# Optimization experiments

Hardware: AMD Instinct MI355X
Metric: run time of the kernel (lower is better)

## Reference

```python
import jax, jax.numpy as jnp
import numpy as np

T_STEPS = 64      # AR order p
MAX_T = 65536     # trajectory length
BATCH = 256       # number of sampled trajectories
STD = 0.3


def setup_inputs() -> dict:
    key = jax.random.key(0)
    k1, k2, k3 = jax.random.split(key, 3)
    raw = jax.random.normal(k1, (T_STEPS,), dtype=jnp.float32)
    # torch init: params / sum(|params|)
    params = raw / jnp.sum(jnp.abs(raw))
    bias = jax.random.uniform(k2, (1,), dtype=jnp.float32)
    noise = jax.random.normal(k3, (BATCH, MAX_T), dtype=jnp.float32)
    return {"params": params, "bias": bias, "noise": noise}


def _ar_means(params, bias, length):
    """AR(p) recurrence: mean_i = sum_k params[k] * x[i-1-k] + bias, x init = 0.
    State holds the last p values, most-recent-first (matches the reversed
    indexing inputs[i-1 : i-p-1 : -1] in the torch code)."""
    p = params.shape[0]

    def step(state, _):
        new = jnp.dot(state, params) + bias[0]
        state = jnp.concatenate([new[None], state[:-1]])
        return state, new

    init = jnp.zeros((p,), dtype=params.dtype)
    _, means = jax.lax.scan(step, init, None, length=length)
    return means  # [length]


def reference(params, bias, noise):
    # means of the Normal over the trajectory (deterministic, shared by batch)
    means = _ar_means(params, bias, noise.shape[1])  # [T]
    # reparameterized sample: actions = mean + std * eps, eps ~ N(0, 1)
    actions = means[None, :] + jnp.asarray(STD, noise.dtype) * noise  # [B, T]
    return actions
```

## Files before the change

### kernel.cpp

```cpp
#include <hip/hip_runtime.h>

#define T_LEN   65536
#define BATCH   256
#define P       64
#define BASE    4096
#define K1_THREADS 256
#define W_TILE  1024
#define BCHUNK  8
#define VOFF    65536

typedef float f4 __attribute__((ext_vector_type(4)));


__constant__ int SCH_DST[14] = { 2, 3, 4, 6, 5, 7, 8,10,12,14, 9,11,13,15};
__constant__ int SCH_SRC[14] = { 1, 2, 2, 3, 4, 6, 4, 5, 6, 7, 8,10,12,14};
__constant__ int SCH_DBL[14] = { 1, 0, 1, 1, 0, 0, 1, 1, 1, 1, 0, 0, 0, 0};
__constant__ int SCH_W[14]   = {192,256,128,192,256,256,64,192,128,192,256,256,256,256};

__global__ __launch_bounds__(K1_THREADS, 1) void ar_k1(const float* __restrict__ params,
                                                       float* __restrict__ R) {
    __shared__ __align__(16) float Rl[BASE];
    __shared__ float p[128];
    __shared__ float Wp[64][4];
    __shared__ __align__(16) float Vs[68];
    __shared__ __align__(16) float Vnode[16][68];
    __shared__ __align__(16) float Tn[8][256];
    __shared__ __align__(16) float Ts[256];
    const int tid = threadIdx.x;
    if (tid < 128) p[tid] = (tid < P) ? params[tid] : 0.f;
    __syncthreads();

    if (tid < 64) {
        float z = 0.f;
        const float pk = p[tid];
        for (int t = 0; t < 64; ++t) {
            float y  = __shfl(z, 0) + 1.0f;
            float zn = __shfl_down(z, 1);
            if (tid == 63) zn = 0.f;
            z = fmaf(pk, y, zn);
            if (tid == 0) Rl[t] = y;
        }
    }
    __syncthreads();

    for (int L = 64; L <= BASE / 2; L <<= 1) {
        {
            const int j = tid >> 2, c = tid & 3;
            const int mbase = c << 4;
            float w = 0.f;
            #pragma unroll
            for (int mm = 0; mm < 16; ++mm) {
                const int m = mbase + mm;
                w = fmaf(p[m + j], Rl[L - 1 - m], w);
            }
            Wp[j][c] = w;
        }
        __syncthreads();
        if (tid <= P) {
            const float wj  = (tid < P)
                ? (Wp[tid][0] + Wp[tid][1] + Wp[tid][2] + Wp[tid][3]) : 0.f;
            const float wm1 = (tid >= 1)
                ? (Wp[tid-1][0] + Wp[tid-1][1] + Wp[tid-1][2] + Wp[tid-1][3]) : 0.f;
            Vs[tid] = wj - wm1;
        }
        __syncthreads();
        if (tid < P) {
            const int tau = tid;
            float acc = Rl[tau];
            #pragma unroll
            for (int i = 0; i < P; ++i) {
                const int idx = (tau - i) > 0 ? (tau - i) : 0;
                const float v = (i <= tau) ? Vs[i] : 0.f;
                acc = fmaf(v, Rl[idx], acc);
            }
            Rl[L + tau] = acc;
        }
        {
            const f4* __restrict__ Rl4 = reinterpret_cast<const f4*>(Rl);
            f4* __restrict__ Rl4w = reinterpret_cast<f4*>(Rl);
            const f4* __restrict__ V4 = reinterpret_cast<const f4*>(Vs);
            const int nq = (L - 64) >> 2;
            #pragma unroll 1
            for (int q = tid; q < nq; q += K1_THREADS) {
                f4 w4[17];
                #pragma unroll
                for (int j = 0; j < 17; ++j) w4[j] = Rl4[q + j];
                float a0 = w4[16].x, a1 = w4[16].y, a2 = w4[16].z, a3 = w4[16].w;
                #pragma unroll
                for (int g = 0; g < 16; ++g) {
                    const f4 v  = V4[g];
                    const f4 hi = w4[16 - g];
                    const f4 lo = w4[15 - g];
                    a0 = fmaf(v.x, hi.x, a0); a1 = fmaf(v.x, hi.y, a1);
                    a2 = fmaf(v.x, hi.z, a2); a3 = fmaf(v.x, hi.w, a3);
                    a0 = fmaf(v.y, lo.w, a0); a1 = fmaf(v.y, hi.x, a1);
                    a2 = fmaf(v.y, hi.y, a2); a3 = fmaf(v.y, hi.z, a3);
                    a0 = fmaf(v.z, lo.z, a0); a1 = fmaf(v.z, lo.w, a1);
                    a2 = fmaf(v.z, hi.x, a2); a3 = fmaf(v.z, hi.y, a3);
                    a0 = fmaf(v.w, lo.y, a0); a1 = fmaf(v.w, lo.z, a1);
                    a2 = fmaf(v.w, lo.w, a2); a3 = fmaf(v.w, hi.x, a3);
                }
                const float v64 = Vs[64];
                a0 = fmaf(v64, w4[0].x, a0); a1 = fmaf(v64, w4[0].y, a1);
                a2 = fmaf(v64, w4[0].z, a2); a3 = fmaf(v64, w4[0].w, a3);
                f4 o; o.x = a0; o.y = a1; o.z = a2; o.w = a3;
                Rl4w[((L + 64) >> 2) + q] = o;
            }
        }
        __syncthreads();
    }

    for (int j = tid; j < BASE / 4; j += K1_THREADS)
        reinterpret_cast<f4*>(R)[j] = reinterpret_cast<const f4*>(Rl)[j];

    Tn[1][tid] = Rl[3840 + tid];
    __syncthreads();
    {
        const int j = tid >> 2, c = tid & 3, mbase = c << 4;
        float w = 0.f;
        #pragma unroll
        for (int mm = 0; mm < 16; ++mm) {
            const int m = mbase + mm;
            w = fmaf(p[m + j], Tn[1][255 - m], w);
        }
        Wp[j][c] = w;
    }
    __syncthreads();
    if (tid <= P) {
        const float wj  = (tid < P)
            ? (Wp[tid][0] + Wp[tid][1] + Wp[tid][2] + Wp[tid][3]) : 0.f;
        const float wm1 = (tid >= 1)
            ? (Wp[tid-1][0] + Wp[tid-1][1] + Wp[tid-1][2] + Wp[tid-1][3]) : 0.f;
        Vnode[1][tid] = wj - wm1;
    }
    __syncthreads();

    for (int s = 0; s < 14; ++s) {
        const int dst = SCH_DST[s], src = SCH_SRC[s], wd = SCH_W[s];
        const bool dbl = SCH_DBL[s] != 0;
        float* td = (dst <= 7) ? Tn[dst] : Ts;
        const float* tsrc = Tn[src];
        const float* Vsr  = Vnode[src];
        if (tid < wd) {
            const float* s0 = dbl ? (tsrc + 64) : (Rl + 3840);
            float acc = s0[tid];
            #pragma unroll
            for (int i = 0; i <= P; ++i)
                acc = fmaf(Vsr[i], s0[tid - i], acc);
            td[tid] = acc;
        }
        __syncthreads();
        {
            const int j = tid >> 2, c = tid & 3, mbase = c << 4;
            float w = 0.f;
            #pragma unroll
            for (int mm = 0; mm < 16; ++mm) {
                const int m = mbase + mm;
                w = fmaf(p[m + j], td[wd - 1 - m], w);
            }
            Wp[j][c] = w;
        }
        __syncthreads();
        if (tid <= P) {
            const float wj  = (tid < P)
                ? (Wp[tid][0] + Wp[tid][1] + Wp[tid][2] + Wp[tid][3]) : 0.f;
            const float wm1 = (tid >= 1)
                ? (Wp[tid-1][0] + Wp[tid-1][1] + Wp[tid-1][2] + Wp[tid-1][3]) : 0.f;
            Vnode[dst][tid] = wj - wm1;
        }
        __syncthreads();
    }

    for (int j = tid; j < 15 * 80; j += K1_THREADS) {
        const int k = j / 80 + 1, i = j - (k - 1) * 80;
        if (i < 65) R[VOFF + k * 80 + i] = Vnode[k][i];
    }
}

__global__ __launch_bounds__(256) void ar_out_fused(const float* __restrict__ R,
                                                    const float* __restrict__ bias,
                                                    const float* __restrict__ noise,
                                                    float* __restrict__ out) {
    __shared__ __align__(16) float win[1088];
    __shared__ __align__(16) float Vl[68];
    const int tid  = threadIdx.x;
    const int tile = blockIdx.x & 63;
    const int bc   = blockIdx.x >> 6;
    const int t0   = tile * W_TILE;
    const float b  = bias[0];
    const int k    = t0 >> 12;
    const f4* __restrict__ Rg4 = reinterpret_cast<const f4*>(R);

    f4 rt;
    if (k == 0) {
        const f4 r = Rg4[(t0 >> 2) + tid];
        rt.x = b * r.x; rt.y = b * r.y; rt.z = b * r.z; rt.w = b * r.w;
    } else {
        const int tau0 = t0 & 4095;
        if (tid < 65) Vl[tid] = R[VOFF + k * 80 + tid];
        f4* __restrict__ win4 = reinterpret_cast<f4*>(win);
        for (int j4 = tid; j4 < 272; j4 += 256) {
            const int u = tau0 - 64 + 4 * j4;
            f4 v;
            if (u >= 0) v = Rg4[u >> 2];
            else { v.x = 0.f; v.y = 0.f; v.z = 0.f; v.w = 0.f; }
            win4[j4] = v;
        }
        __syncthreads();
        const f4* __restrict__ V4 = reinterpret_cast<const f4*>(Vl);
        f4 w4[17];
        #pragma unroll
        for (int j = 0; j < 17; ++j) w4[j] = win4[tid + j];
        float a0 = w4[16].x, a1 = w4[16].y, a2 = w4[16].z, a3 = w4[16].w;
        #pragma unroll
        for (int g = 0; g < 16; ++g) {
            const f4 v  = V4[g];
            const f4 hi = w4[16 - g];
            const f4 lo = w4[15 - g];
            a0 = fmaf(v.x, hi.x, a0); a1 = fmaf(v.x, hi.y, a1);
            a2 = fmaf(v.x, hi.z, a2); a3 = fmaf(v.x, hi.w, a3);
            a0 = fmaf(v.y, lo.w, a0); a1 = fmaf(v.y, hi.x, a1);
            a2 = fmaf(v.y, hi.y, a2); a3 = fmaf(v.y, hi.z, a3);
            a0 = fmaf(v.z, lo.z, a0); a1 = fmaf(v.z, lo.w, a1);
            a2 = fmaf(v.z, hi.x, a2); a3 = fmaf(v.z, hi.y, a3);
            a0 = fmaf(v.w, lo.y, a0); a1 = fmaf(v.w, lo.z, a1);
            a2 = fmaf(v.w, lo.w, a2); a3 = fmaf(v.w, hi.x, a3);
        }
        const float v64 = Vl[64];
        a0 = fmaf(v64, w4[0].x, a0); a1 = fmaf(v64, w4[0].y, a1);
        a2 = fmaf(v64, w4[0].z, a2); a3 = fmaf(v64, w4[0].w, a3);
        rt.x = b * a0; rt.y = b * a1; rt.z = b * a2; rt.w = b * a3;
    }

    const int nb4 = T_LEN >> 2;
    const int col = (t0 >> 2) + tid;
    const f4* __restrict__ n4 = reinterpret_cast<const f4*>(noise);
    f4* __restrict__ o4 = reinterpret_cast<f4*>(out);
    #pragma unroll
    for (int bi = 0; bi < BCHUNK; ++bi) {
        const int idx = (bc * BCHUNK + bi) * nb4 + col;
        const f4 n = __builtin_nontemporal_load(n4 + idx);
        f4 o;
        o.x = fmaf(0.3f, n.x, rt.x);
        o.y = fmaf(0.3f, n.y, rt.y);
        o.z = fmaf(0.3f, n.z, rt.z);
        o.w = fmaf(0.3f, n.w, rt.w);
        __builtin_nontemporal_store(o, o4 + idx);
    }
}

extern "C" void kernel_launch(void* const* d_in, const int* in_sizes, int n_in,
                              void* d_out, int out_size, void* d_ws, size_t ws_size,
                              hipStream_t stream) {
    const float* params = (const float*)d_in[0];
    const float* bias   = (const float*)d_in[1];
    const float* noise  = (const float*)d_in[2];
    float* out = (float*)d_out;
    float* R   = (float*)d_ws;

    hipLaunchKernelGGL(ar_k1, dim3(1), dim3(K1_THREADS), 0, stream, params, R);
    hipLaunchKernelGGL(ar_out_fused, dim3(64 * 32), dim3(256), 0, stream,
                       R, bias, noise, out);
}
```

Measured before the change: 166.3 us.

## Fuse AR prefix and output kernels into one cooperative launch with grid sync

Merges the single-block AR coefficient kernel and the streaming output kernel into one cooperative kernel of 512 blocks. Block 0 computes the recurrence tables while every other block prefetches 16 rows of noise into registers. All blocks then meet at a grid-wide sync and each writes 32 batch rows. The aim is to hide the serial recurrence behind noise loads and drop a kernel launch boundary. The costs are grid-sync overhead, higher register pressure from holding 16 float4 values per thread, and a fallback to the old two-kernel path if the cooperative launch fails.

```diff
diff --git a/kernel.cpp b/kernel.cpp
--- a/kernel.cpp
+++ b/kernel.cpp
@@ -1,12 +1,13 @@
 #include <hip/hip_runtime.h>
+#include <hip/hip_cooperative_groups.h>
+
+namespace cg = cooperative_groups;
 
 #define T_LEN   65536
 #define BATCH   256
 #define P       64
 #define BASE    4096
-#define K1_THREADS 256
 #define W_TILE  1024
-#define BCHUNK  8
 #define VOFF    65536
 
 typedef float f4 __attribute__((ext_vector_type(4)));
@@ -17,15 +18,11 @@
 __constant__ int SCH_DBL[14] = { 1, 0, 1, 1, 0, 0, 1, 1, 1, 1, 0, 0, 0, 0};
 __constant__ int SCH_W[14]   = {192,256,128,192,256,256,64,192,128,192,256,256,256,256};
 
-__global__ __launch_bounds__(K1_THREADS, 1) void ar_k1(const float* __restrict__ params,
-                                                       float* __restrict__ R) {
-    __shared__ __align__(16) float Rl[BASE];
-    __shared__ float p[128];
-    __shared__ float Wp[64][4];
-    __shared__ __align__(16) float Vs[68];
-    __shared__ __align__(16) float Vnode[16][68];
-    __shared__ __align__(16) float Tn[8][256];
-    __shared__ __align__(16) float Ts[256];
+__device__ __forceinline__ void k1_body(const float* __restrict__ params,
+                                        float* __restrict__ R,
+                                        float* Rl, float* p, float (*Wp)[4],
+                                        float* Vs, float (*Vnode)[68],
+                                        float (*Tn)[256], float* Ts) {
     const int tid = threadIdx.x;
     if (tid < 128) p[tid] = (tid < P) ? params[tid] : 0.f;
     __syncthreads();
@@ -81,7 +78,7 @@
             const f4* __restrict__ V4 = reinterpret_cast<const f4*>(Vs);
             const int nq = (L - 64) >> 2;
             #pragma unroll 1
-            for (int q = tid; q < nq; q += K1_THREADS) {
+            for (int q = tid; q < nq; q += 256) {
                 f4 w4[17];
                 #pragma unroll
                 for (int j = 0; j < 17; ++j) w4[j] = Rl4[q + j];
@@ -110,7 +107,7 @@
         __syncthreads();
     }
 
-    for (int j = tid; j < BASE / 4; j += K1_THREADS)
+    for (int j = tid; j < BASE / 4; j += 256)
         reinterpret_cast<f4*>(R)[j] = reinterpret_cast<const f4*>(Rl)[j];
 
     Tn[1][tid] = Rl[3840 + tid];
@@ -171,26 +168,17 @@
         __syncthreads();
     }
 
-    for (int j = tid; j < 15 * 80; j += K1_THREADS) {
+    for (int j = tid; j < 15 * 80; j += 256) {
         const int k = j / 80 + 1, i = j - (k - 1) * 80;
         if (i < 65) R[VOFF + k * 80 + i] = Vnode[k][i];
     }
 }
 
-__global__ __launch_bounds__(256) void ar_out_fused(const float* __restrict__ R,
-                                                    const float* __restrict__ bias,
-                                                    const float* __restrict__ noise,
-                                                    float* __restrict__ out) {
-    __shared__ __align__(16) float win[1088];
-    __shared__ __align__(16) float Vl[68];
-    const int tid  = threadIdx.x;
-    const int tile = blockIdx.x & 63;
-    const int bc   = blockIdx.x >> 6;
-    const int t0   = tile * W_TILE;
-    const float b  = bias[0];
-    const int k    = t0 >> 12;
+__device__ __forceinline__ f4 tile_rt(const float* __restrict__ R, int t0,
+                                      float b, float* win, float* Vl) {
+    const int tid = threadIdx.x;
+    const int k   = t0 >> 12;
     const f4* __restrict__ Rg4 = reinterpret_cast<const f4*>(R);
-
     f4 rt;
     if (k == 0) {
         const f4 r = Rg4[(t0 >> 2) + tid];
@@ -231,14 +219,116 @@
         a2 = fmaf(v64, w4[0].z, a2); a3 = fmaf(v64, w4[0].w, a3);
         rt.x = b * a0; rt.y = b * a1; rt.z = b * a2; rt.w = b * a3;
     }
-
+    return rt;
+}
+
+__global__ __launch_bounds__(256, 2) void ar_fused(const float* __restrict__ params,
+                                                   const float* __restrict__ bias,
+                                                   const float* __restrict__ noise,
+                                                   float* __restrict__ out,
+                                                   float* __restrict__ R) {
+    __shared__ __align__(16) float Rl[BASE];
+    __shared__ float p[128];
+    __shared__ float Wp[64][4];
+    __shared__ __align__(16) float Vs[68];
+    __shared__ __align__(16) float Vnode[16][68];
+    __shared__ __align__(16) float Tn[8][256];
+    __shared__ __align__(16) float Ts[256];
+    __shared__ __align__(16) float win[1088];
+    __shared__ __align__(16) float Vl[68];
+
+    const int tid  = threadIdx.x;
+    const int bid  = blockIdx.x;
+    const int tile = bid & 63;
+    const int bc   = bid >> 6;
+    const int t0   = tile * W_TILE;
+    const float b  = bias[0];
+    const int nb4  = T_LEN >> 2;
+    const int col  = (t0 >> 2) + tid;
+    const f4* __restrict__ n4 = reinterpret_cast<const f4*>(noise);
+    f4* __restrict__ o4 = reinterpret_cast<f4*>(out);
+    const int row0 = bc * 32;
+
+    f4 nf[16];
+    if (bid != 0) {
+        #pragma unroll
+        for (int r = 0; r < 16; ++r)
+            nf[r] = __builtin_nontemporal_load(n4 + ((row0 + r) * nb4 + col));
+    }
+
+    if (bid == 0) {
+        k1_body(params, R, Rl, p, Wp, Vs, Vnode, Tn, Ts);
+        __threadfence();
+    }
+    cg::this_grid().sync();
+
+    const f4 rt = tile_rt(R, t0, b, win, Vl);
+
+    if (bid != 0) {
+        #pragma unroll
+        for (int r = 0; r < 16; ++r) {
+            const f4 n = nf[r];
+            f4 o;
+            o.x = fmaf(0.3f, n.x, rt.x);
+            o.y = fmaf(0.3f, n.y, rt.y);
+            o.z = fmaf(0.3f, n.z, rt.z);
+            o.w = fmaf(0.3f, n.w, rt.w);
+            __builtin_nontemporal_store(o, o4 + ((row0 + r) * nb4 + col));
+        }
+    } else {
+        #pragma unroll 4
+        for (int r = 0; r < 16; ++r) {
+            const f4 n = __builtin_nontemporal_load(n4 + ((row0 + r) * nb4 + col));
+            f4 o;
+            o.x = fmaf(0.3f, n.x, rt.x);
+            o.y = fmaf(0.3f, n.y, rt.y);
+            o.z = fmaf(0.3f, n.z, rt.z);
+            o.w = fmaf(0.3f, n.w, rt.w);
+            __builtin_nontemporal_store(o, o4 + ((row0 + r) * nb4 + col));
+        }
+    }
+    #pragma unroll 4
+    for (int r = 16; r < 32; ++r) {
+        const f4 n = __builtin_nontemporal_load(n4 + ((row0 + r) * nb4 + col));
+        f4 o;
+        o.x = fmaf(0.3f, n.x, rt.x);
+        o.y = fmaf(0.3f, n.y, rt.y);
+        o.z = fmaf(0.3f, n.z, rt.z);
+        o.w = fmaf(0.3f, n.w, rt.w);
+        __builtin_nontemporal_store(o, o4 + ((row0 + r) * nb4 + col));
+    }
+}
+
+__global__ __launch_bounds__(256, 1) void ar_k1(const float* __restrict__ params,
+                                                float* __restrict__ R) {
+    __shared__ __align__(16) float Rl[BASE];
+    __shared__ float p[128];
+    __shared__ float Wp[64][4];
+    __shared__ __align__(16) float Vs[68];
+    __shared__ __align__(16) float Vnode[16][68];
+    __shared__ __align__(16) float Tn[8][256];
+    __shared__ __align__(16) float Ts[256];
+    k1_body(params, R, Rl, p, Wp, Vs, Vnode, Tn, Ts);
+}
+
+__global__ __launch_bounds__(256) void ar_out(const float* __restrict__ R,
+                                              const float* __restrict__ bias,
+                                              const float* __restrict__ noise,
+                                              float* __restrict__ out) {
+    __shared__ __align__(16) float win[1088];
+    __shared__ __align__(16) float Vl[68];
+    const int tid  = threadIdx.x;
+    const int tile = blockIdx.x & 63;
+    const int bc   = blockIdx.x >> 6;
+    const int t0   = tile * W_TILE;
+    const f4 rt = tile_rt(R, t0, bias[0], win, Vl);
     const int nb4 = T_LEN >> 2;
     const int col = (t0 >> 2) + tid;
     const f4* __restrict__ n4 = reinterpret_cast<const f4*>(noise);
     f4* __restrict__ o4 = reinterpret_cast<f4*>(out);
     #pragma unroll
-    for (int bi = 0; bi < BCHUNK; ++bi) {
-        const int idx = (bc * BCHUNK + bi) * nb4 + col;
+    for (int bi = 0; bi < 8; ++bi) {
+        const int idx = (bc * 8 + bi) * nb4 + col;
         const f4 n = __builtin_nontemporal_load(n4 + idx);
         f4 o;
         o.x = fmaf(0.3f, n.x, rt.x);
@@ -247,6 +337,7 @@
         o.w = fmaf(0.3f, n.w, rt.w);
         __builtin_nontemporal_store(o, o4 + idx);
     }
+    (void)tid;
 }
 
 extern "C" void kernel_launch(void* const* d_in, const int* in_sizes, int n_in,
@@ -258,7 +349,15 @@
     float* out = (float*)d_out;
     float* R   = (float*)d_ws;
 
-    hipLaunchKernelGGL(ar_k1, dim3(1), dim3(K1_THREADS), 0, stream, params, R);
-    hipLaunchKernelGGL(ar_out_fused, dim3(64 * 32), dim3(256), 0, stream,
-                       R, bias, noise, out);
-}
+    void* args[] = { (void*)&params, (void*)&bias, (void*)&noise,
+                     (void*)&out, (void*)&R };
+    hipError_t e = hipLaunchCooperativeKernel((const void*)ar_fused,
+                                              dim3(512), dim3(256),
+                                              args, 0, stream);
+    if (e != hipSuccess) {
+        (void)hipGetLastError();
+        hipLaunchKernelGGL(ar_k1, dim3(1), dim3(256), 0, stream, params, R);
+        hipLaunchKernelGGL(ar_out, dim3(64 * 32), dim3(256), 0, stream,
+                           R, bias, noise, out);
+    }
+}
```

After: 276.2 us. 66.1% more time.
